# Kernel optimization log

Hardware: AMD Instinct MI355X
Metric: run time of the kernel (lower is better)

Reference implementation:

```python
import jax, jax.numpy as jnp
import numpy as np

D_MODEL = 1024
NUM_HEADS = 16
HEAD_DIM = D_MODEL // NUM_HEADS
ROPE_BASE = 10000.0


def _rotate_half(x):
    x1, x2 = jnp.split(x, 2, axis=-1)
    return jnp.concatenate([-x2, x1], axis=-1)


def _rope_cache(seq_len, head_dim, dtype):
    half = head_dim // 2
    inv_freq = 1.0 / (ROPE_BASE ** (jnp.arange(half, dtype=jnp.float32) / float(half)))
    t = jnp.arange(seq_len, dtype=jnp.float32)
    freqs = t[:, None] * inv_freq[None, :]          # [s, half]
    emb = jnp.concatenate([freqs, freqs], axis=-1)   # [s, head_dim]
    cos = jnp.cos(emb)[None, None, :, :].astype(dtype)  # [1,1,s,d]
    sin = jnp.sin(emb)[None, None, :, :].astype(dtype)
    return cos, sin


def setup_inputs() -> dict:
    key = jax.random.key(0)
    k1, k2, k3 = jax.random.split(key, 3)
    b, s = 4, 2048
    x = jax.random.normal(k1, (b, s, D_MODEL), dtype=jnp.float32)
    mask = jnp.ones((b, s), dtype=jnp.float32)
    Wqkv = jax.random.normal(k2, (D_MODEL, 3 * D_MODEL), dtype=jnp.float32) * (D_MODEL ** -0.5)
    Wout = jax.random.normal(k3, (D_MODEL, D_MODEL), dtype=jnp.float32) * (D_MODEL ** -0.5)
    return {"x": x, "mask": mask, "Wqkv": Wqkv, "Wout": Wout}


def reference(x, mask, Wqkv, Wout):
    b, s, _ = x.shape
    qkv = x @ Wqkv                                   # [b,s,3*d_model]
    q, k, v = jnp.split(qkv, 3, axis=-1)

    def split_heads(t):
        return t.reshape(b, s, NUM_HEADS, HEAD_DIM).transpose(0, 2, 1, 3)  # [b,h,s,d]

    q, k, v = map(split_heads, (q, k, v))
    cos, sin = _rope_cache(s, HEAD_DIM, x.dtype)
    q = q * cos + _rotate_half(q) * sin
    k = k * cos + _rotate_half(k) * sin

    scale = HEAD_DIM ** -0.5
    logits = jnp.einsum('bhid,bhjd->bhij', q, k) * scale
    logits = logits + (1.0 - mask)[:, None, None, :] * -1e9
    attn = jax.nn.softmax(logits, axis=-1)
    out = jnp.einsum('bhij,bhjd->bhid', attn, v)     # [b,h,s,d]
    out = out.transpose(0, 2, 1, 3).reshape(b, s, D_MODEL)
    return out @ Wout
```

## Files before the change

kernel.cpp:

```cpp
#include <hip/hip_runtime.h>

typedef unsigned short u16;
typedef unsigned int u32;
typedef int i32x2 __attribute__((ext_vector_type(2)));
typedef float f32x4 __attribute__((ext_vector_type(4)));
typedef float f32x16 __attribute__((ext_vector_type(16)));
typedef __bf16 bf16x8 __attribute__((ext_vector_type(8)));
typedef unsigned short u16x8 __attribute__((ext_vector_type(8)));
typedef unsigned short u16x4 __attribute__((ext_vector_type(4)));
typedef unsigned int u32x4 __attribute__((ext_vector_type(4)));

#define S_ 2048
#define DM 1024

#define LDS_U32(p) ((__attribute__((address_space(3))) unsigned int*)(p))
#define GLB_U32(p) ((const __attribute__((address_space(1))) unsigned int*)(p))

__device__ __forceinline__ u16 f2bf(float f) {
    unsigned int u = __float_as_uint(f);
    u += 0x7fffu + ((u >> 16) & 1u);
    return (u16)(u >> 16);
}
__device__ __forceinline__ float bf2f(u16 s) {
    return __uint_as_float(((unsigned int)s) << 16);
}
__device__ __forceinline__ float fast_exp2(float x) {
#if __has_builtin(__builtin_amdgcn_exp2f)
    return __builtin_amdgcn_exp2f(x);
#else
    return __expf(x * 0.69314718056f);
#endif
}

__global__ __launch_bounds__(256) void f32_to_bf16_kernel(const float* __restrict__ in,
                                                          u16* __restrict__ o, int n) {
    int i = (blockIdx.x * 256 + threadIdx.x) << 2;
    if (i >= n) return;
    float4 f = *(const float4*)&in[i];
    u16x4 r;
    r[0] = f2bf(f.x); r[1] = f2bf(f.y); r[2] = f2bf(f.z); r[3] = f2bf(f.w);
    *(u16x4*)&o[i] = r;
}

__global__ __launch_bounds__(256) void transpose_w(const float* __restrict__ W,
                                                   u16* __restrict__ Wt, int K, int N) {
    __shared__ float tile[32][33];
    int nb = blockIdx.x << 5, kb = blockIdx.y << 5;
    int tx = threadIdx.x & 31, ty = threadIdx.x >> 5;
#pragma unroll
    for (int r = 0; r < 32; r += 8)
        tile[ty + r][tx] = W[(size_t)(kb + ty + r) * N + nb + tx];
    __syncthreads();
#pragma unroll
    for (int r = 0; r < 32; r += 8)
        Wt[(size_t)(nb + ty + r) * K + kb + tx] = f2bf(tile[tx][ty + r]);
}


#define ABLK(B, KK) ((B) * 24576 + (KK) * 4096)
#define BBLK(B, KK) ((B) * 24576 + 8192 + (KK) * 8192)

template <int MODE>
__global__ __launch_bounds__(512, 2) void gemm256(const u16* __restrict__ A,
                                                  const u16* __restrict__ Bt,
                                                  float* __restrict__ Cf,
                                                  u16* __restrict__ Qp, u16* __restrict__ Kp,
                                                  u16* __restrict__ Vtp,
                                                  int M, int N, int K) {
    __shared__ __align__(16) u16 lds[49152];
    const int tid = threadIdx.x, wave = tid >> 6, lane = tid & 63;
    const int Ntiles = N >> 8;
    const int cpx = gridDim.x >> 3;
    const int bid = (int)blockIdx.x;
    const int wg = (bid & 7) * cpx + (bid >> 3);
    const int mt = wg / Ntiles, nt = wg % Ntiles;
    const int m0 = mt << 7, n0 = nt << 8;
    const int wm = (wave >> 2) << 6, wn = (wave & 3) << 6;
    const int lr = lane & 15, lu = lane >> 4;

    const int NT = K >> 6;
    const int NIT = K >> 7;

    f32x4 acc[4][4] = {};

    const int srow0 = wave * 16 + (lane >> 2);
    const int scole = (((lane & 3) ^ ((lane >> 3) & 3)) << 3);

#define STAGE_A(BLK, KCOL)                                                                \
    {                                                                                     \
        const u16* src = &A[(size_t)(m0 + srow0) * K + (KCOL) + scole];                   \
        __builtin_amdgcn_global_load_lds(GLB_U32(src),                                    \
            LDS_U32(&lds[(BLK) + wave * 512]), 16, 0, 0);                                 \
    }
#define STAGE_B(BLK, KCOL)                                                                \
    {                                                                                     \
        _Pragma("unroll") for (int l = 0; l < 2; ++l) {                                   \
            const u16* src = &Bt[(size_t)(n0 + srow0 + l * 128) * K + (KCOL) + scole];    \
            __builtin_amdgcn_global_load_lds(GLB_U32(src),                                \
                LDS_U32(&lds[(BLK) + l * 4096 + wave * 512]), 16, 0, 0);                  \
        }                                                                                 \
    }

#define LDFRAG(BLK, ROW) \
    __builtin_bit_cast(bf16x8, *(const u16x8*)&lds[(BLK) + (ROW) * 32 + ((lu ^ (((ROW) >> 1) & 3)) << 3)])

#define PHASE(BUF, KK, SBUF, SKK, SKT)                                                    \
    {                                                                                     \
        _Pragma("unroll") for (int ii = 0; ii < 4; ++ii)                                  \
            af[ii] = LDFRAG(ABLK(BUF, KK), wm + ii * 16 + lr);                            \
        _Pragma("unroll") for (int j = 0; j < 4; ++j)                                     \
            bfv[j] = LDFRAG(BBLK(BUF, KK), wn + j * 16 + lr);                             \
        {                                                                                 \
            const int kcol = (((SKT) & (NT - 1)) << 6) + ((SKK) << 5);                    \
            STAGE_A(ABLK(SBUF, SKK), kcol);                                               \
            STAGE_B(BBLK(SBUF, SKK), kcol);                                               \
        }                                                                                 \
        asm volatile("s_barrier" ::: "memory");                                           \
        asm volatile("s_waitcnt lgkmcnt(0)" ::: "memory");                                \
        __builtin_amdgcn_sched_barrier(0);                                                \
        __builtin_amdgcn_s_setprio(1);                                                    \
        _Pragma("unroll") for (int ii = 0; ii < 4; ++ii)                                  \
            _Pragma("unroll") for (int j = 0; j < 4; ++j)                                 \
                acc[ii][j] = __builtin_amdgcn_mfma_f32_16x16x32_bf16(                     \
                    af[ii], bfv[j], acc[ii][j], 0, 0, 0);                                 \
        __builtin_amdgcn_s_setprio(0);                                                    \
        asm volatile("s_waitcnt vmcnt(6)" ::: "memory");                                  \
        asm volatile("s_barrier" ::: "memory");                                           \
    }

    STAGE_A(ABLK(0, 0), 0);
    STAGE_B(BBLK(0, 0), 0);
    STAGE_A(ABLK(0, 1), 32);
    STAGE_B(BBLK(0, 1), 32);
    STAGE_A(ABLK(1, 0), 64);
    STAGE_B(BBLK(1, 0), 64);
    asm volatile("s_waitcnt vmcnt(6)" ::: "memory");
    asm volatile("s_barrier" ::: "memory");

    for (int t = 0; t < NIT; ++t) {
        const int kt = 2 * t;
        bf16x8 af[4], bfv[4];
        PHASE(0, 0, 1, 1, kt + 1);
        PHASE(0, 1, 0, 0, kt + 2);
        PHASE(1, 0, 0, 1, kt + 2);
        PHASE(1, 1, 1, 0, kt + 3);
    }

    if (MODE == 0) {
        const int t = (n0 + wn) >> 10;
        if (t < 2) {
            const float LN1E4_32 = 9.210340371976184f / 32.0f;
            const float invf0 = __expf(-(float)lr * LN1E4_32);
            const float invf1 = __expf(-(float)(lr + 16) * LN1E4_32);
#pragma unroll
            for (int i = 0; i < 4; ++i) {
                const int rbase = m0 + wm + (i << 4) + ((lane >> 4) << 2);
#pragma unroll
                for (int jj = 0; jj < 4; ++jj) {
                    const float s = (float)((rbase + jj) & (S_ - 1));
                    float sn0, c0, sn1, c1;
                    __sincosf(s * invf0, &sn0, &c0);
                    __sincosf(s * invf1, &sn1, &c1);
                    const float v0 = acc[i][0][jj], v1 = acc[i][1][jj];
                    const float v2 = acc[i][2][jj], v3 = acc[i][3][jj];
                    acc[i][0][jj] = v0 * c0 - v2 * sn0;
                    acc[i][2][jj] = v2 * c0 + v0 * sn0;
                    acc[i][1][jj] = v1 * c1 - v3 * sn1;
                    acc[i][3][jj] = v3 * c1 + v1 * sn1;
                }
            }
            u16* P = (t == 0) ? Qp : Kp;
#pragma unroll
            for (int i = 0; i < 4; ++i) {
#pragma unroll
                for (int j = 0; j < 4; ++j) {
                    int rbase = m0 + wm + (i << 4) + ((lane >> 4) << 2);
                    int col = n0 + wn + (j << 4) + lr;
                    int h = (col & 1023) >> 6, d = col & 63;
#pragma unroll
                    for (int jj = 0; jj < 4; ++jj) {
                        int row = rbase + jj;
                        int b = row >> 11, s = row & 2047;
                        P[((size_t)((b << 4) + h) * S_ + s) * 64 + d] = f2bf(acc[i][j][jj]);
                    }
                }
            }
        } else {
#pragma unroll
            for (int i = 0; i < 4; ++i) {
                const int rbase = m0 + wm + (i << 4) + ((lane >> 4) << 2);
                const int b = rbase >> 11, sb = rbase & 2047;
#pragma unroll
                for (int j = 0; j < 4; ++j) {
                    int col = n0 + wn + (j << 4) + lr;
                    int h = (col & 1023) >> 6, d = col & 63;
                    u16x4 pk;
#pragma unroll
                    for (int jj = 0; jj < 4; ++jj) pk[jj] = f2bf(acc[i][j][jj]);
                    *(u16x4*)&Vtp[((size_t)((b << 4) + h) * 64 + d) * S_ + sb] = pk;
                }
            }
        }
    } else {
#pragma unroll
        for (int i = 0; i < 4; ++i)
#pragma unroll
            for (int j = 0; j < 4; ++j) {
                int rbase = m0 + wm + (i << 4) + ((lane >> 4) << 2);
                int col = n0 + wn + (j << 4) + lr;
#pragma unroll
                for (int jj = 0; jj < 4; ++jj)
                    Cf[(size_t)(rbase + jj) * N + col] = acc[i][j][jj];
            }
    }
#undef PHASE
#undef LDFRAG
#undef STAGE_B
#undef STAGE_A
}

__device__ __forceinline__ void softmax_chain(f32x16* p, u32* wa, u32* wb,
                                              const float* madd_tile, bool hasmask,
                                              int hi) {
    if (hasmask) {
#pragma unroll
        for (int tt = 0; tt < 2; ++tt)
#pragma unroll
            for (int rq = 0; rq < 4; ++rq) {
                float4 mf = *(const float4*)&madd_tile[tt * 32 + rq * 8 + hi * 4];
                p[tt][4 * rq + 0] += mf.x;
                p[tt][4 * rq + 1] += mf.y;
                p[tt][4 * rq + 2] += mf.z;
                p[tt][4 * rq + 3] += mf.w;
            }
    }

#pragma unroll
    for (int tt = 0; tt < 2; ++tt)
#pragma unroll
        for (int r = 0; r < 16; ++r)
            p[tt][r] = fast_exp2(p[tt][r]);

#pragma unroll
    for (int tt = 0; tt < 2; ++tt)
#pragma unroll
        for (int rq = 0; rq < 4; ++rq) {
            float e0 = p[tt][4 * rq + 0], e1 = p[tt][4 * rq + 1];
            float e2 = p[tt][4 * rq + 2], e3 = p[tt][4 * rq + 3];
            u32 w0, w1;
            asm("v_cvt_pk_bf16_f32 %0, %1, %2" : "=v"(w0) : "v"(e0), "v"(e1));
            asm("v_cvt_pk_bf16_f32 %0, %1, %2" : "=v"(w1) : "v"(e2), "v"(e3));
            wa[4 * tt + rq] = w0;
            wb[4 * tt + rq] = w1;
        }
}

__global__ __launch_bounds__(256, 2) void attn_kernel(const u16* __restrict__ q,
                                                      const u16* __restrict__ k,
                                                      const u16* __restrict__ vt,
                                                      const float* __restrict__ mask,
                                                      u16* __restrict__ outp) {
    __shared__ __align__(16) u16 Kl[2][64 * 64];
    __shared__ __align__(16) u16 Vl[2][64 * 64];
    __shared__ float madd2[2][64];

    const int tid = threadIdx.x, wave = tid >> 6, lane = tid & 63;
    const int c = lane & 31, hi = lane >> 5, c7 = c & 7;
    const int bh = blockIdx.x & 63, qt = blockIdx.x >> 6;
    const int b = bh >> 4, h = bh & 15;
    const size_t base = (size_t)bh * (S_ * 64);
    const int qrowA = (qt << 8) + (wave << 5) + c;
    const int qrowB = qrowA + 128;

    const float QS = 0.18033688f;

    bf16x8 qfA[4], qfB[4];
#pragma unroll
    for (int j = 0; j < 4; ++j) {
        u16x8 rawA = *(const u16x8*)&q[base + (size_t)qrowA * 64 + j * 16 + hi * 8];
        u16x8 rawB = *(const u16x8*)&q[base + (size_t)qrowB * 64 + j * 16 + hi * 8];
        u16x8 scA, scB;
#pragma unroll
        for (int e = 0; e < 8; ++e) {
            scA[e] = f2bf(bf2f(rawA[e]) * QS);
            scB[e] = f2bf(bf2f(rawB[e]) * QS);
        }
        qfA[j] = __builtin_bit_cast(bf16x8, scA);
        qfB[j] = __builtin_bit_cast(bf16x8, scB);
    }

    u16x8 ou;
#pragma unroll
    for (int e = 0; e < 8; ++e) ou[e] = 0x3F80;
    const bf16x8 onesf = __builtin_bit_cast(bf16x8, ou);

    f32x16 accA[2] = {}, accB[2] = {};
    f32x16 accSA = {}, accSB = {};

    const int sr = tid >> 2, su = (tid & 3) << 1;
    const int so0 = sr * 64 + ((su ^ (sr & 7)) << 3);
    const int so1 = sr * 64 + (((su + 1) ^ (sr & 7)) << 3);

    u16x8 kc0 = *(const u16x8*)&k[base + (size_t)sr * 64 + su * 8];
    u16x8 kc1 = *(const u16x8*)&k[base + (size_t)sr * 64 + su * 8 + 8];
    u16x8 vc0 = *(const u16x8*)&vt[base + (size_t)sr * S_ + su * 8];
    u16x8 vc1 = *(const u16x8*)&vt[base + (size_t)sr * S_ + su * 8 + 8];
    float mval = (tid < 64) ? mask[b * S_ + tid] : 1.0f;

    for (int t = 0; t < 32; ++t) {
        const int bi = t & 1;
        u16* Kb = &Kl[bi][0];
        u16* Vb = &Vl[bi][0];
        *(u16x8*)&Kb[so0] = kc0;
        *(u16x8*)&Kb[so1] = kc1;
        *(u16x8*)&Vb[so0] = vc0;
        *(u16x8*)&Vb[so1] = vc1;
        if (tid < 64) madd2[bi][tid] = (1.0f - mval) * -1.44269504e9f;
        if (t + 1 < 32) {
            const int kn = (t + 1) << 6;
            kc0 = *(const u16x8*)&k[base + (size_t)(kn + sr) * 64 + su * 8];
            kc1 = *(const u16x8*)&k[base + (size_t)(kn + sr) * 64 + su * 8 + 8];
            vc0 = *(const u16x8*)&vt[base + (size_t)sr * S_ + kn + su * 8];
            vc1 = *(const u16x8*)&vt[base + (size_t)sr * S_ + kn + su * 8 + 8];
            mval = (tid < 64) ? mask[b * S_ + kn + tid] : 1.0f;
        }
        __syncthreads();

        f32x16 pA[2] = {}, pB[2] = {};
        __builtin_amdgcn_s_setprio(1);
#pragma unroll
        for (int j = 0; j < 4; ++j) {
            const int uo = ((2 * j + hi) ^ c7) << 3;
            bf16x8 ka  = __builtin_bit_cast(bf16x8, *(const u16x8*)&Kb[c * 64 + uo]);
            bf16x8 kb2 = __builtin_bit_cast(bf16x8, *(const u16x8*)&Kb[(32 + c) * 64 + uo]);
            pA[0] = __builtin_amdgcn_mfma_f32_32x32x16_bf16(ka,  qfA[j], pA[0], 0, 0, 0);
            pA[1] = __builtin_amdgcn_mfma_f32_32x32x16_bf16(kb2, qfA[j], pA[1], 0, 0, 0);
            pB[0] = __builtin_amdgcn_mfma_f32_32x32x16_bf16(ka,  qfB[j], pB[0], 0, 0, 0);
            pB[1] = __builtin_amdgcn_mfma_f32_32x32x16_bf16(kb2, qfB[j], pB[1], 0, 0, 0);
        }
        __builtin_amdgcn_s_setprio(0);

        bool hasmask = __any(madd2[bi][lane] != 0.0f);

        u32 waA[8], wbA[8], waB[8], wbB[8];
        softmax_chain(pA, waA, wbA, &madd2[bi][0], hasmask, hi);
        softmax_chain(pB, waB, wbB, &madd2[bi][0], hasmask, hi);

        __builtin_amdgcn_s_setprio(1);
#pragma unroll
        for (int ks = 0; ks < 4; ++ks) {
            i32x2 raA = __builtin_amdgcn_permlane32_swap((int)waA[2 * ks], (int)waA[2 * ks + 1], false, false);
            i32x2 rbA = __builtin_amdgcn_permlane32_swap((int)wbA[2 * ks], (int)wbA[2 * ks + 1], false, false);
            i32x2 raB = __builtin_amdgcn_permlane32_swap((int)waB[2 * ks], (int)waB[2 * ks + 1], false, false);
            i32x2 rbB = __builtin_amdgcn_permlane32_swap((int)wbB[2 * ks], (int)wbB[2 * ks + 1], false, false);
            u32x4 pwA, pwB;
            pwA[0] = (u32)raA[0]; pwA[1] = (u32)rbA[0]; pwA[2] = (u32)raA[1]; pwA[3] = (u32)rbA[1];
            pwB[0] = (u32)raB[0]; pwB[1] = (u32)rbB[0]; pwB[2] = (u32)raB[1]; pwB[3] = (u32)rbB[1];
            bf16x8 pafA = __builtin_bit_cast(bf16x8, pwA);
            bf16x8 pafB = __builtin_bit_cast(bf16x8, pwB);
            accSA = __builtin_amdgcn_mfma_f32_32x32x16_bf16(pafA, onesf, accSA, 0, 0, 0);
            accSB = __builtin_amdgcn_mfma_f32_32x32x16_bf16(pafB, onesf, accSB, 0, 0, 0);
            const int uo = ((2 * ks + hi) ^ c7) << 3;
#pragma unroll
            for (int dt = 0; dt < 2; ++dt) {
                bf16x8 vf = __builtin_bit_cast(bf16x8,
                            *(const u16x8*)&Vb[(32 * dt + c) * 64 + uo]);
                accA[dt] = __builtin_amdgcn_mfma_f32_32x32x16_bf16(pafA, vf, accA[dt], 0, 0, 0);
                accB[dt] = __builtin_amdgcn_mfma_f32_32x32x16_bf16(pafB, vf, accB[dt], 0, 0, 0);
            }
        }
        __builtin_amdgcn_s_setprio(0);
    }

    {
        const size_t orow0 = (size_t)b * S_ + (qt << 8) + (wave << 5);
#pragma unroll
        for (int dt = 0; dt < 2; ++dt)
#pragma unroll
            for (int r = 0; r < 16; ++r) {
                int qr = (r & 3) + 8 * (r >> 2) + 4 * hi;
                outp[(orow0 + qr) * DM + h * 64 + dt * 32 + c] =
                    f2bf(accA[dt][r] * __builtin_amdgcn_rcpf(accSA[r]));
            }
    }
    {
        const size_t orow0 = (size_t)b * S_ + (qt << 8) + (wave << 5) + 128;
#pragma unroll
        for (int dt = 0; dt < 2; ++dt)
#pragma unroll
            for (int r = 0; r < 16; ++r) {
                int qr = (r & 3) + 8 * (r >> 2) + 4 * hi;
                outp[(orow0 + qr) * DM + h * 64 + dt * 32 + c] =
                    f2bf(accB[dt][r] * __builtin_amdgcn_rcpf(accSB[r]));
            }
    }
}

extern "C" void kernel_launch(void* const* d_in, const int* in_sizes, int n_in,
                              void* d_out, int out_size, void* d_ws, size_t ws_size,
                              hipStream_t stream) {
    const float* x    = (const float*)d_in[0];
    const float* mask = (const float*)d_in[1];
    const float* Wqkv = (const float*)d_in[2];
    const float* Wout = (const float*)d_in[3];
    float* out = (float*)d_out;
    char* ws = (char*)d_ws;
    const size_t MB = 1u << 20;
    u16* xb    = (u16*)(ws);
    u16* WqkvT = (u16*)(ws + 16 * MB);
    u16* WoutT = (u16*)(ws + 22 * MB);
    u16* qb    = (u16*)(ws + 24 * MB);
    u16* kb    = (u16*)(ws + 40 * MB);
    u16* vtb   = (u16*)(ws + 56 * MB);
    u16* ao    = xb;

    f32_to_bf16_kernel<<<8192, 256, 0, stream>>>(x, xb, 8192 * 1024);
    transpose_w<<<dim3(96, 32), 256, 0, stream>>>(Wqkv, WqkvT, 1024, 3072);
    transpose_w<<<dim3(32, 32), 256, 0, stream>>>(Wout, WoutT, 1024, 1024);
    gemm256<0><<<64 * 12, 512, 0, stream>>>(xb, WqkvT, nullptr, qb, kb, vtb, 8192, 3072, 1024);
    attn_kernel<<<512, 256, 0, stream>>>(qb, kb, vtb, mask, ao);
    gemm256<1><<<64 * 4, 512, 0, stream>>>(ao, WoutT, out, nullptr, nullptr, nullptr, 8192, 1024, 1024);
}
```

Measured before the change: 190.0 us.

## Split attention query tile across eight waves instead of two rows per wave

The attention kernel now launches 512 threads per block, and each wave processes one 32-row query tile instead of two (A and B). K/V tile staging is spread over twice as many threads, so each thread loads one 16-byte chunk per tile instead of two. This roughly halves per-thread register pressure and raises the number of resident waves, which helps latency hiding. In exchange, K/V LDS fragments are reused across only one query tile per wave, so LDS reads per MFMA increase, and more waves share each block barrier.

```diff
diff --git a/kernel.cpp b/kernel.cpp
--- a/kernel.cpp
+++ b/kernel.cpp
@@ -255,7 +255,7 @@
         }
 }
 
-__global__ __launch_bounds__(256, 2) void attn_kernel(const u16* __restrict__ q,
+__global__ __launch_bounds__(512, 4) void attn_kernel(const u16* __restrict__ q,
                                                       const u16* __restrict__ k,
                                                       const u16* __restrict__ vt,
                                                       const float* __restrict__ mask,
@@ -269,24 +269,18 @@
     const int bh = blockIdx.x & 63, qt = blockIdx.x >> 6;
     const int b = bh >> 4, h = bh & 15;
     const size_t base = (size_t)bh * (S_ * 64);
-    const int qrowA = (qt << 8) + (wave << 5) + c;
-    const int qrowB = qrowA + 128;
+    const int qrow = (qt << 8) + (wave << 5) + c;
 
     const float QS = 0.18033688f;
 
-    bf16x8 qfA[4], qfB[4];
+    bf16x8 qf[4];
 #pragma unroll
     for (int j = 0; j < 4; ++j) {
-        u16x8 rawA = *(const u16x8*)&q[base + (size_t)qrowA * 64 + j * 16 + hi * 8];
-        u16x8 rawB = *(const u16x8*)&q[base + (size_t)qrowB * 64 + j * 16 + hi * 8];
-        u16x8 scA, scB;
-#pragma unroll
-        for (int e = 0; e < 8; ++e) {
-            scA[e] = f2bf(bf2f(rawA[e]) * QS);
-            scB[e] = f2bf(bf2f(rawB[e]) * QS);
-        }
-        qfA[j] = __builtin_bit_cast(bf16x8, scA);
-        qfB[j] = __builtin_bit_cast(bf16x8, scB);
+        u16x8 raw = *(const u16x8*)&q[base + (size_t)qrow * 64 + j * 16 + hi * 8];
+        u16x8 sc;
+#pragma unroll
+        for (int e = 0; e < 8; ++e) sc[e] = f2bf(bf2f(raw[e]) * QS);
+        qf[j] = __builtin_bit_cast(bf16x8, sc);
     }
 
     u16x8 ou;
@@ -294,79 +288,66 @@
     for (int e = 0; e < 8; ++e) ou[e] = 0x3F80;
     const bf16x8 onesf = __builtin_bit_cast(bf16x8, ou);
 
-    f32x16 accA[2] = {}, accB[2] = {};
-    f32x16 accSA = {}, accSB = {};
-
-    const int sr = tid >> 2, su = (tid & 3) << 1;
-    const int so0 = sr * 64 + ((su ^ (sr & 7)) << 3);
-    const int so1 = sr * 64 + (((su + 1) ^ (sr & 7)) << 3);
-
-    u16x8 kc0 = *(const u16x8*)&k[base + (size_t)sr * 64 + su * 8];
-    u16x8 kc1 = *(const u16x8*)&k[base + (size_t)sr * 64 + su * 8 + 8];
-    u16x8 vc0 = *(const u16x8*)&vt[base + (size_t)sr * S_ + su * 8];
-    u16x8 vc1 = *(const u16x8*)&vt[base + (size_t)sr * S_ + su * 8 + 8];
+    f32x16 acc[2] = {};
+    f32x16 accS = {};
+
+    const int sr = tid >> 3, su = tid & 7;
+    const int so = sr * 64 + ((su ^ (sr & 7)) << 3);
+
+    u16x8 kc = *(const u16x8*)&k[base + (size_t)sr * 64 + su * 8];
+    u16x8 vc = *(const u16x8*)&vt[base + (size_t)sr * S_ + su * 8];
     float mval = (tid < 64) ? mask[b * S_ + tid] : 1.0f;
 
     for (int t = 0; t < 32; ++t) {
         const int bi = t & 1;
         u16* Kb = &Kl[bi][0];
         u16* Vb = &Vl[bi][0];
-        *(u16x8*)&Kb[so0] = kc0;
-        *(u16x8*)&Kb[so1] = kc1;
-        *(u16x8*)&Vb[so0] = vc0;
-        *(u16x8*)&Vb[so1] = vc1;
+        *(u16x8*)&Kb[so] = kc;
+        *(u16x8*)&Vb[so] = vc;
         if (tid < 64) madd2[bi][tid] = (1.0f - mval) * -1.44269504e9f;
         if (t + 1 < 32) {
             const int kn = (t + 1) << 6;
-            kc0 = *(const u16x8*)&k[base + (size_t)(kn + sr) * 64 + su * 8];
-            kc1 = *(const u16x8*)&k[base + (size_t)(kn + sr) * 64 + su * 8 + 8];
-            vc0 = *(const u16x8*)&vt[base + (size_t)sr * S_ + kn + su * 8];
-            vc1 = *(const u16x8*)&vt[base + (size_t)sr * S_ + kn + su * 8 + 8];
+            kc = *(const u16x8*)&k[base + (size_t)(kn + sr) * 64 + su * 8];
+            vc = *(const u16x8*)&vt[base + (size_t)sr * S_ + kn + su * 8];
             mval = (tid < 64) ? mask[b * S_ + kn + tid] : 1.0f;
         }
         __syncthreads();
 
-        f32x16 pA[2] = {}, pB[2] = {};
+        f32x16 p[2] = {};
         __builtin_amdgcn_s_setprio(1);
 #pragma unroll
         for (int j = 0; j < 4; ++j) {
             const int uo = ((2 * j + hi) ^ c7) << 3;
             bf16x8 ka  = __builtin_bit_cast(bf16x8, *(const u16x8*)&Kb[c * 64 + uo]);
             bf16x8 kb2 = __builtin_bit_cast(bf16x8, *(const u16x8*)&Kb[(32 + c) * 64 + uo]);
-            pA[0] = __builtin_amdgcn_mfma_f32_32x32x16_bf16(ka,  qfA[j], pA[0], 0, 0, 0);
-            pA[1] = __builtin_amdgcn_mfma_f32_32x32x16_bf16(kb2, qfA[j], pA[1], 0, 0, 0);
-            pB[0] = __builtin_amdgcn_mfma_f32_32x32x16_bf16(ka,  qfB[j], pB[0], 0, 0, 0);
-            pB[1] = __builtin_amdgcn_mfma_f32_32x32x16_bf16(kb2, qfB[j], pB[1], 0, 0, 0);
+            p[0] = __builtin_amdgcn_mfma_f32_32x32x16_bf16(ka,  qf[j], p[0], 0, 0, 0);
+            p[1] = __builtin_amdgcn_mfma_f32_32x32x16_bf16(kb2, qf[j], p[1], 0, 0, 0);
         }
         __builtin_amdgcn_s_setprio(0);
 
         bool hasmask = __any(madd2[bi][lane] != 0.0f);
 
-        u32 waA[8], wbA[8], waB[8], wbB[8];
-        softmax_chain(pA, waA, wbA, &madd2[bi][0], hasmask, hi);
-        softmax_chain(pB, waB, wbB, &madd2[bi][0], hasmask, hi);
+        u32 wa[8], wb[8];
+        softmax_chain(p, wa, wb, &madd2[bi][0], hasmask, hi);
 
         __builtin_amdgcn_s_setprio(1);
 #pragma unroll
         for (int ks = 0; ks < 4; ++ks) {
-            i32x2 raA = __builtin_amdgcn_permlane32_swap((int)waA[2 * ks], (int)waA[2 * ks + 1], false, false);
-            i32x2 rbA = __builtin_amdgcn_permlane32_swap((int)wbA[2 * ks], (int)wbA[2 * ks + 1], false, false);
-            i32x2 raB = __builtin_amdgcn_permlane32_swap((int)waB[2 * ks], (int)waB[2 * ks + 1], false, false);
-            i32x2 rbB = __builtin_amdgcn_permlane32_swap((int)wbB[2 * ks], (int)wbB[2 * ks + 1], false, false);
-            u32x4 pwA, pwB;
-            pwA[0] = (u32)raA[0]; pwA[1] = (u32)rbA[0]; pwA[2] = (u32)raA[1]; pwA[3] = (u32)rbA[1];
-            pwB[0] = (u32)raB[0]; pwB[1] = (u32)rbB[0]; pwB[2] = (u32)raB[1]; pwB[3] = (u32)rbB[1];
-            bf16x8 pafA = __builtin_bit_cast(bf16x8, pwA);
-            bf16x8 pafB = __builtin_bit_cast(bf16x8, pwB);
-            accSA = __builtin_amdgcn_mfma_f32_32x32x16_bf16(pafA, onesf, accSA, 0, 0, 0);
-            accSB = __builtin_amdgcn_mfma_f32_32x32x16_bf16(pafB, onesf, accSB, 0, 0, 0);
+            i32x2 ra = __builtin_amdgcn_permlane32_swap((int)wa[2 * ks], (int)wa[2 * ks + 1], false, false);
+            i32x2 rb = __builtin_amdgcn_permlane32_swap((int)wb[2 * ks], (int)wb[2 * ks + 1], false, false);
+            u32x4 pw;
+            pw[0] = (u32)ra[0];
+            pw[1] = (u32)rb[0];
+            pw[2] = (u32)ra[1];
+            pw[3] = (u32)rb[1];
+            bf16x8 paf = __builtin_bit_cast(bf16x8, pw);
+            accS = __builtin_amdgcn_mfma_f32_32x32x16_bf16(paf, onesf, accS, 0, 0, 0);
             const int uo = ((2 * ks + hi) ^ c7) << 3;
 #pragma unroll
             for (int dt = 0; dt < 2; ++dt) {
                 bf16x8 vf = __builtin_bit_cast(bf16x8,
                             *(const u16x8*)&Vb[(32 * dt + c) * 64 + uo]);
-                accA[dt] = __builtin_amdgcn_mfma_f32_32x32x16_bf16(pafA, vf, accA[dt], 0, 0, 0);
-                accB[dt] = __builtin_amdgcn_mfma_f32_32x32x16_bf16(pafB, vf, accB[dt], 0, 0, 0);
+                acc[dt] = __builtin_amdgcn_mfma_f32_32x32x16_bf16(paf, vf, acc[dt], 0, 0, 0);
             }
         }
         __builtin_amdgcn_s_setprio(0);
@@ -380,18 +361,7 @@
             for (int r = 0; r < 16; ++r) {
                 int qr = (r & 3) + 8 * (r >> 2) + 4 * hi;
                 outp[(orow0 + qr) * DM + h * 64 + dt * 32 + c] =
-                    f2bf(accA[dt][r] * __builtin_amdgcn_rcpf(accSA[r]));
-            }
-    }
-    {
-        const size_t orow0 = (size_t)b * S_ + (qt << 8) + (wave << 5) + 128;
-#pragma unroll
-        for (int dt = 0; dt < 2; ++dt)
-#pragma unroll
-            for (int r = 0; r < 16; ++r) {
-                int qr = (r & 3) + 8 * (r >> 2) + 4 * hi;
-                outp[(orow0 + qr) * DM + h * 64 + dt * 32 + c] =
-                    f2bf(accB[dt][r] * __builtin_amdgcn_rcpf(accSB[r]));
+                    f2bf(acc[dt][r] * __builtin_amdgcn_rcpf(accS[r]));
             }
     }
 }
@@ -418,6 +388,6 @@
     transpose_w<<<dim3(96, 32), 256, 0, stream>>>(Wqkv, WqkvT, 1024, 3072);
     transpose_w<<<dim3(32, 32), 256, 0, stream>>>(Wout, WoutT, 1024, 1024);
     gemm256<0><<<64 * 12, 512, 0, stream>>>(xb, WqkvT, nullptr, qb, kb, vtb, 8192, 3072, 1024);
-    attn_kernel<<<512, 256, 0, stream>>>(qb, kb, vtb, mask, ao);
+    attn_kernel<<<512, 512, 0, stream>>>(qb, kb, vtb, mask, ao);
     gemm256<1><<<64 * 4, 512, 0, stream>>>(ao, WoutT, out, nullptr, nullptr, nullptr, 8192, 1024, 1024);
 }
```

After: 200.2 us. 1.05x slower.
